# Kernel optimization log

Hardware: AMD Instinct MI355X
Metric: run time of the kernel (lower is better)

Reference implementation:

```python
import jax, jax.numpy as jnp
import numpy as np

RADIUS = 51  # odd-ified from 50
WEIGHT = 0.5
THRESHOLD = 10.0


def _gaussian_kernel_2d(k: int) -> np.ndarray:
    # Replicates cv2.getGaussianKernel(k, 0): sigma = 0.3*((k-1)*0.5 - 1) + 0.8
    sigma = 0.3 * ((k - 1) * 0.5 - 1.0) + 0.8
    x = np.arange(k, dtype=np.float64) - (k - 1) / 2.0
    g = np.exp(-(x ** 2) / (2.0 * sigma ** 2))
    g = g / g.sum()
    return np.outer(g, g).astype(np.float32)  # (k, k)


def filter2d(img, kernel):
    # img: (b, c, h, w), kernel: (k, k); depthwise 'same' conv (symmetric zero pad)
    b, c, h, w = img.shape
    k = kernel.shape[-1]
    p = k // 2
    x = img.reshape(b * c, 1, h, w)
    w2 = kernel.reshape(1, 1, k, k).astype(img.dtype)
    out = jax.lax.conv_general_dilated(
        x, w2,
        window_strides=(1, 1),
        padding=[(p, p), (p, p)],
        dimension_numbers=("NCHW", "OIHW", "NCHW"),
    )
    return out.reshape(b, c, h, w)


def setup_inputs() -> dict:
    key = jax.random.key(0)
    img = jax.random.uniform(key, (16, 3, 512, 512), dtype=jnp.float32)
    kernel = jnp.asarray(_gaussian_kernel_2d(RADIUS))
    return {"img": img, "kernel": kernel}


def reference(img, kernel):
    blur = filter2d(img, kernel)
    residual = img - blur
    mask = (jnp.abs(residual) * 255.0 > THRESHOLD).astype(img.dtype)
    soft_mask = filter2d(mask, kernel)
    sharp = jnp.clip(img + WEIGHT * residual, 0.0, 1.0)
    return soft_mask * sharp + (1.0 - soft_mask) * img
```

## Files before the change

kernel.cpp:

```cpp
#include <hip/hip_runtime.h>
#include <hip/hip_fp16.h>
#include <math.h>

#define IMG_H 512
#define IMG_W 512
#define NCH   48
#define KR    51
#define WEIGHT 0.5f
#define MASK_BITS 0x2905

typedef _Float16 f16x8 __attribute__((ext_vector_type(8)));
typedef float    f32x4 __attribute__((ext_vector_type(4)));

struct GK { float g[KR]; };

__device__ __forceinline__ f16x8 band_frag(const unsigned short* tbl, int delta,
                                           int lane) {
  union { f16x8 v; unsigned short s[8]; } r;
  const int base = delta + 63 - (lane & 15) + 4 * (lane >> 4);
  #pragma unroll
  for (int e = 0; e < 8; ++e)
    r.s[e] = tbl[base + (e & 3) + 16 * (e >> 2)];
  return r.v;
}

__device__ __forceinline__ int swz1536(int b) { return (b & 7) * 192 + (b >> 3); }

template <int MODE>
__global__ __launch_bounds__(256) void hpass(const void* __restrict__ inp,
                                             __half* __restrict__ outp, GK gk) {
  __shared__ unsigned short tbl[128];
  const int tid = threadIdx.x;
  if (tid < 128) {
    int j = tid - 38;
    float v = (j >= 0 && j < KR) ? gk.g[j] : 0.f;
    tbl[tid] = __half_as_ushort(__float2half(v));
  }
  __syncthreads();
  const int lane = tid & 63;
  const int w    = tid >> 6;
  const int r0   = blockIdx.x * 16;
  const int x0   = w * 128;
  const int row  = r0 + (lane & 15);
  const int g4   = 4 * (lane >> 4);

  f16x8 bf[6];
  #pragma unroll
  for (int d = 0; d < 6; ++d) bf[d] = band_frag(tbl, 16 * d - 48, lane);

  f32x4 acc[8];
  #pragma unroll
  for (int n = 0; n < 8; ++n) acc[n] = (f32x4){0.f, 0.f, 0.f, 0.f};

  #pragma unroll
  for (int n = 0; n < 8; ++n) {
    #pragma unroll
    for (int i = 0; i < 3; ++i) {
      const int D  = 32 * (((16 * n - 25) >> 5) + i) - 16 * n;
      const int kb = x0 + 16 * n + D;
      if (kb >= 0 && kb < IMG_W) {
        union { f16x8 v; _Float16 h[8]; unsigned short s[8]; } a;
        if (MODE == 0) {
          const float* pr = (const float*)inp + (size_t)row * IMG_W + kb + g4;
          float4 lo = *reinterpret_cast<const float4*>(pr);
          float4 hi = *reinterpret_cast<const float4*>(pr + 16);
          a.h[0] = (_Float16)lo.x; a.h[1] = (_Float16)lo.y;
          a.h[2] = (_Float16)lo.z; a.h[3] = (_Float16)lo.w;
          a.h[4] = (_Float16)hi.x; a.h[5] = (_Float16)hi.y;
          a.h[6] = (_Float16)hi.z; a.h[7] = (_Float16)hi.w;
        } else {
          const unsigned short* pr =
              (const unsigned short*)inp + (size_t)row * IMG_W + kb + g4;
          uint2 lo = *reinterpret_cast<const uint2*>(pr);
          uint2 hi = *reinterpret_cast<const uint2*>(pr + 16);
          unsigned short sv[8] = {
            (unsigned short)(lo.x), (unsigned short)(lo.x >> 16),
            (unsigned short)(lo.y), (unsigned short)(lo.y >> 16),
            (unsigned short)(hi.x), (unsigned short)(hi.x >> 16),
            (unsigned short)(hi.y), (unsigned short)(hi.y >> 16) };
          #pragma unroll
          for (int e = 0; e < 8; ++e)
            a.s[e] = ((sv[e] & 0x7fff) > MASK_BITS) ? 0x3C00 : 0;
        }
        const int bi = (n & 1) ? 2 * i : 2 * i + 1;
        acc[n] = __builtin_amdgcn_mfma_f32_16x16x32_f16(a.v, bf[bi], acc[n],
                                                        0, 0, 0);
      }
    }
  }
  const int q = 4 * (lane >> 4);
  #pragma unroll
  for (int n = 0; n < 8; ++n) {
    const int col = x0 + 16 * n + (lane & 15);
    #pragma unroll
    for (int j = 0; j < 4; ++j)
      outp[(size_t)(r0 + q + j) * IMG_W + col] = __float2half(acc[n][j]);
  }
}

template <int FINAL>
__global__ __launch_bounds__(256) void vpass(const __half* __restrict__ tin,
                                             const float* __restrict__ img,
                                             const __half* __restrict__ resv,
                                             void* __restrict__ outp, GK gk) {
  __shared__ unsigned short tbl[128];
  const int tid = threadIdx.x;
  if (tid < 128) {
    int j = tid - 38;
    float v = (j >= 0 && j < KR) ? gk.g[j] : 0.f;
    tbl[tid] = __half_as_ushort(__float2half(v));
  }
  __syncthreads();
  const int lane = tid & 63;
  const int w    = tid >> 6;
  const int b    = swz1536(blockIdx.x);
  const int c    = b >> 5;
  const int yb   = (b >> 2) & 7;
  const int xb   = b & 3;
  const int ybw  = yb * 64 + 32 * (w >> 1);
  const int x0   = xb * 128 + 64 * (w & 1);
  const size_t plane = (size_t)c * IMG_H * IMG_W;

  f16x8 bf[6];
  #pragma unroll
  for (int d = 0; d < 6; ++d) bf[d] = band_frag(tbl, 16 * d - 48, lane);

  f32x4 acc[2][4];
  #pragma unroll
  for (int yt = 0; yt < 2; ++yt)
    #pragma unroll
    for (int xt = 0; xt < 4; ++xt) acc[yt][xt] = (f32x4){0.f, 0.f, 0.f, 0.f};

  const int g4 = 4 * (lane >> 4);
  #pragma unroll
  for (int xt = 0; xt < 4; ++xt) {
    const int colg = x0 + 16 * xt + (lane & 15);
    #pragma unroll
    for (int i = 0; i < 3; ++i) {
      const int k0 = ybw + 32 * (i - 1);
      if (k0 >= 0 && k0 < IMG_H) {
        const unsigned short* pB =
            (const unsigned short*)tin + plane + (size_t)(k0 + g4) * IMG_W + colg;
        union { f16x8 v; unsigned short s[8]; } bv;
        #pragma unroll
        for (int e = 0; e < 8; ++e)
          bv.s[e] = pB[(size_t)((e & 3) + 16 * (e >> 2)) * IMG_W];
        acc[0][xt] = __builtin_amdgcn_mfma_f32_16x16x32_f16(bf[2 * i + 1], bv.v,
                                                            acc[0][xt], 0, 0, 0);
        acc[1][xt] = __builtin_amdgcn_mfma_f32_16x16x32_f16(bf[2 * i],     bv.v,
                                                            acc[1][xt], 0, 0, 0);
      }
    }
  }
  #pragma unroll
  for (int yt = 0; yt < 2; ++yt) {
    #pragma unroll
    for (int xt = 0; xt < 4; ++xt) {
      const int y0 = ybw + 16 * yt + g4;
      const int xc = x0 + 16 * xt + (lane & 15);
      #pragma unroll
      for (int j = 0; j < 4; ++j) {
        const size_t off = plane + (size_t)(y0 + j) * IMG_W + xc;
        const float bl = acc[yt][xt][j];
        const float iv = img[off];
        if (FINAL) {
          const float r = __half2float(resv[off]);
          const float sharp = fminf(fmaxf(fmaf(WEIGHT, r, iv), 0.f), 1.f);
          ((float*)outp)[off] = fmaf(bl, sharp - iv, iv);
        } else {
          ((__half*)outp)[off] = __float2half(iv - bl);
        }
      }
    }
  }
}

extern "C" void kernel_launch(void* const* d_in, const int* in_sizes, int n_in,
                              void* d_out, int out_size, void* d_ws, size_t ws_size,
                              hipStream_t stream) {
  const float* img = (const float*)d_in[0];
  GK gk;
  {
    double sigma = 0.3 * ((KR - 1) * 0.5 - 1.0) + 0.8;
    double gs[KR], sum = 0.0;
    for (int i = 0; i < KR; ++i) {
      double xd = (double)i - (KR - 1) / 2.0;
      gs[i] = exp(-(xd * xd) / (2.0 * sigma * sigma));
      sum += gs[i];
    }
    for (int i = 0; i < KR; ++i) gk.g[i] = (float)(gs[i] / sum);
  }

  const size_t npx = (size_t)NCH * IMG_H * IMG_W;
  __half* t1  = (__half*)d_out;
  __half* res = (__half*)d_ws;
  __half* t2  = (__half*)((char*)d_ws + npx * sizeof(__half));

  const int hgrid = NCH * IMG_H / 16;
  const int vgrid = NCH * (IMG_H / 64) * (IMG_W / 128);

  hpass<0><<<hgrid, 256, 0, stream>>>(img, t1, gk);
  vpass<0><<<vgrid, 256, 0, stream>>>(t1, img, res , res, gk);
  hpass<1><<<hgrid, 256, 0, stream>>>(res, t2, gk);
  vpass<1><<<vgrid, 256, 0, stream>>>(t2, img, res, d_out, gk);
}
```

Measured before the change: 207.1 us.

## Fuse horizontal and vertical blur passes into one kernel per stage

Merges the separable horizontal and vertical MFMA passes into a single kernel per blur stage. Each wave computes horizontal blur for a 128-row halo strip of a 16-column slice, keeps the fp16 results in registers, and feeds them directly as the B operand of the vertical MFMA. This removes the intermediate t1/t2 global round-trips and two launches. In exchange, each tile recomputes horizontal blur over the vertical halo (128 rows for 64 output rows), roughly doubling horizontal MFMA work and input reads.

```diff
diff --git a/kernel.cpp b/kernel.cpp
--- a/kernel.cpp
+++ b/kernel.cpp
@@ -10,6 +10,7 @@
 #define MASK_BITS 0x2905
 
 typedef _Float16 f16x8 __attribute__((ext_vector_type(8)));
+typedef _Float16 f16x4 __attribute__((ext_vector_type(4)));
 typedef float    f32x4 __attribute__((ext_vector_type(4)));
 
 struct GK { float g[KR]; };
@@ -24,11 +25,12 @@
   return r.v;
 }
 
-__device__ __forceinline__ int swz1536(int b) { return (b & 7) * 192 + (b >> 3); }
+__device__ __forceinline__ int swz3072(int b) { return (b & 7) * 384 + (b >> 3); }
 
-template <int MODE>
-__global__ __launch_bounds__(256) void hpass(const void* __restrict__ inp,
-                                             __half* __restrict__ outp, GK gk) {
+template <int PASS>
+__global__ __launch_bounds__(256) void fusedhv(const float* __restrict__ img,
+                                               const __half* __restrict__ resv,
+                                               void* __restrict__ outp, GK gk) {
   __shared__ unsigned short tbl[128];
   const int tid = threadIdx.x;
   if (tid < 128) {
@@ -37,139 +39,108 @@
     tbl[tid] = __half_as_ushort(__float2half(v));
   }
   __syncthreads();
+
   const int lane = tid & 63;
   const int w    = tid >> 6;
-  const int r0   = blockIdx.x * 16;
-  const int x0   = w * 128;
-  const int row  = r0 + (lane & 15);
-  const int g4   = 4 * (lane >> 4);
+  const int b    = swz3072(blockIdx.x);
+  const int c    = b >> 6;
+  const int yb   = (b >> 3) & 7;
+  const int xb   = b & 7;
+  const int y0   = yb * 64;
+  const int xw   = xb * 64 + 16 * w;
+  const size_t plane = (size_t)c * IMG_H * IMG_W;
+  const int l15 = lane & 15;
+  const int g4  = 4 * (lane >> 4);
 
   f16x8 bf[6];
   #pragma unroll
   for (int d = 0; d < 6; ++d) bf[d] = band_frag(tbl, 16 * d - 48, lane);
 
-  f32x4 acc[8];
+  const bool podd = (xw >> 4) & 1;
+  f16x8 bh[3];
   #pragma unroll
-  for (int n = 0; n < 8; ++n) acc[n] = (f32x4){0.f, 0.f, 0.f, 0.f};
+  for (int i = 0; i < 3; ++i) bh[i] = podd ? bf[2 * i] : bf[2 * i + 1];
+
+  const int kb0 = ((xw - 25) >> 5) * 32;
+
+  f16x4 h16[8];
+  #pragma unroll
+  for (int ch = 0; ch < 8; ++ch) {
+    f32x4 acc = {0.f, 0.f, 0.f, 0.f};
+    const int r0 = y0 - 32 + 16 * ch;
+    if (r0 >= 0 && r0 < IMG_H) {
+      const size_t rowoff = plane + (size_t)(r0 + l15) * IMG_W;
+      #pragma unroll
+      for (int i = 0; i < 3; ++i) {
+        const int kb = kb0 + 32 * i;
+        if (kb >= 0 && kb < IMG_W) {
+          union { f16x8 v; _Float16 h[8]; unsigned short s[8]; } a;
+          if (PASS == 0) {
+            const float* pr = img + rowoff + kb + g4;
+            float4 lo = *reinterpret_cast<const float4*>(pr);
+            float4 hi = *reinterpret_cast<const float4*>(pr + 16);
+            a.h[0] = (_Float16)lo.x; a.h[1] = (_Float16)lo.y;
+            a.h[2] = (_Float16)lo.z; a.h[3] = (_Float16)lo.w;
+            a.h[4] = (_Float16)hi.x; a.h[5] = (_Float16)hi.y;
+            a.h[6] = (_Float16)hi.z; a.h[7] = (_Float16)hi.w;
+          } else {
+            const unsigned short* pr =
+                (const unsigned short*)resv + rowoff + kb + g4;
+            uint2 lo = *reinterpret_cast<const uint2*>(pr);
+            uint2 hi = *reinterpret_cast<const uint2*>(pr + 16);
+            unsigned short sv[8] = {
+              (unsigned short)lo.x, (unsigned short)(lo.x >> 16),
+              (unsigned short)lo.y, (unsigned short)(lo.y >> 16),
+              (unsigned short)hi.x, (unsigned short)(hi.x >> 16),
+              (unsigned short)hi.y, (unsigned short)(hi.y >> 16) };
+            #pragma unroll
+            for (int e = 0; e < 8; ++e)
+              a.s[e] = ((sv[e] & 0x7fff) > MASK_BITS) ? 0x3C00 : 0;
+          }
+          acc = __builtin_amdgcn_mfma_f32_16x16x32_f16(a.v, bh[i], acc, 0, 0, 0);
+        }
+      }
+    }
+    f16x4 hq;
+    hq[0] = (_Float16)acc[0]; hq[1] = (_Float16)acc[1];
+    hq[2] = (_Float16)acc[2]; hq[3] = (_Float16)acc[3];
+    h16[ch] = hq;
+  }
+
+  f32x4 accv[4];
+  #pragma unroll
+  for (int yc = 0; yc < 4; ++yc) accv[yc] = (f32x4){0.f, 0.f, 0.f, 0.f};
+  #pragma unroll
+  for (int yc = 0; yc < 4; ++yc) {
+    #pragma unroll
+    for (int i = 0; i < 3; ++i) {
+      const int kr = ((16 * yc - 25) >> 5) + i;
+      const int ci = 2 * kr + 2;
+      union { f16x8 v; f16x4 q[2]; } bv;
+      bv.q[0] = h16[ci]; bv.q[1] = h16[ci + 1];
+      if (yc & 1)
+        accv[yc] = __builtin_amdgcn_mfma_f32_16x16x32_f16(bf[2 * i], bv.v,
+                                                          accv[yc], 0, 0, 0);
+      else
+        accv[yc] = __builtin_amdgcn_mfma_f32_16x16x32_f16(bf[2 * i + 1], bv.v,
+                                                          accv[yc], 0, 0, 0);
+    }
+  }
 
   #pragma unroll
-  for (int n = 0; n < 8; ++n) {
+  for (int yc = 0; yc < 4; ++yc) {
     #pragma unroll
-    for (int i = 0; i < 3; ++i) {
-      const int D  = 32 * (((16 * n - 25) >> 5) + i) - 16 * n;
-      const int kb = x0 + 16 * n + D;
-      if (kb >= 0 && kb < IMG_W) {
-        union { f16x8 v; _Float16 h[8]; unsigned short s[8]; } a;
-        if (MODE == 0) {
-          const float* pr = (const float*)inp + (size_t)row * IMG_W + kb + g4;
-          float4 lo = *reinterpret_cast<const float4*>(pr);
-          float4 hi = *reinterpret_cast<const float4*>(pr + 16);
-          a.h[0] = (_Float16)lo.x; a.h[1] = (_Float16)lo.y;
-          a.h[2] = (_Float16)lo.z; a.h[3] = (_Float16)lo.w;
-          a.h[4] = (_Float16)hi.x; a.h[5] = (_Float16)hi.y;
-          a.h[6] = (_Float16)hi.z; a.h[7] = (_Float16)hi.w;
-        } else {
-          const unsigned short* pr =
-              (const unsigned short*)inp + (size_t)row * IMG_W + kb + g4;
-          uint2 lo = *reinterpret_cast<const uint2*>(pr);
-          uint2 hi = *reinterpret_cast<const uint2*>(pr + 16);
-          unsigned short sv[8] = {
-            (unsigned short)(lo.x), (unsigned short)(lo.x >> 16),
-            (unsigned short)(lo.y), (unsigned short)(lo.y >> 16),
-            (unsigned short)(hi.x), (unsigned short)(hi.x >> 16),
-            (unsigned short)(hi.y), (unsigned short)(hi.y >> 16) };
-          #pragma unroll
-          for (int e = 0; e < 8; ++e)
-            a.s[e] = ((sv[e] & 0x7fff) > MASK_BITS) ? 0x3C00 : 0;
-        }
-        const int bi = (n & 1) ? 2 * i : 2 * i + 1;
-        acc[n] = __builtin_amdgcn_mfma_f32_16x16x32_f16(a.v, bf[bi], acc[n],
-                                                        0, 0, 0);
-      }
-    }
-  }
-  const int q = 4 * (lane >> 4);
-  #pragma unroll
-  for (int n = 0; n < 8; ++n) {
-    const int col = x0 + 16 * n + (lane & 15);
-    #pragma unroll
-    for (int j = 0; j < 4; ++j)
-      outp[(size_t)(r0 + q + j) * IMG_W + col] = __float2half(acc[n][j]);
-  }
-}
-
-template <int FINAL>
-__global__ __launch_bounds__(256) void vpass(const __half* __restrict__ tin,
-                                             const float* __restrict__ img,
-                                             const __half* __restrict__ resv,
-                                             void* __restrict__ outp, GK gk) {
-  __shared__ unsigned short tbl[128];
-  const int tid = threadIdx.x;
-  if (tid < 128) {
-    int j = tid - 38;
-    float v = (j >= 0 && j < KR) ? gk.g[j] : 0.f;
-    tbl[tid] = __half_as_ushort(__float2half(v));
-  }
-  __syncthreads();
-  const int lane = tid & 63;
-  const int w    = tid >> 6;
-  const int b    = swz1536(blockIdx.x);
-  const int c    = b >> 5;
-  const int yb   = (b >> 2) & 7;
-  const int xb   = b & 3;
-  const int ybw  = yb * 64 + 32 * (w >> 1);
-  const int x0   = xb * 128 + 64 * (w & 1);
-  const size_t plane = (size_t)c * IMG_H * IMG_W;
-
-  f16x8 bf[6];
-  #pragma unroll
-  for (int d = 0; d < 6; ++d) bf[d] = band_frag(tbl, 16 * d - 48, lane);
-
-  f32x4 acc[2][4];
-  #pragma unroll
-  for (int yt = 0; yt < 2; ++yt)
-    #pragma unroll
-    for (int xt = 0; xt < 4; ++xt) acc[yt][xt] = (f32x4){0.f, 0.f, 0.f, 0.f};
-
-  const int g4 = 4 * (lane >> 4);
-  #pragma unroll
-  for (int xt = 0; xt < 4; ++xt) {
-    const int colg = x0 + 16 * xt + (lane & 15);
-    #pragma unroll
-    for (int i = 0; i < 3; ++i) {
-      const int k0 = ybw + 32 * (i - 1);
-      if (k0 >= 0 && k0 < IMG_H) {
-        const unsigned short* pB =
-            (const unsigned short*)tin + plane + (size_t)(k0 + g4) * IMG_W + colg;
-        union { f16x8 v; unsigned short s[8]; } bv;
-        #pragma unroll
-        for (int e = 0; e < 8; ++e)
-          bv.s[e] = pB[(size_t)((e & 3) + 16 * (e >> 2)) * IMG_W];
-        acc[0][xt] = __builtin_amdgcn_mfma_f32_16x16x32_f16(bf[2 * i + 1], bv.v,
-                                                            acc[0][xt], 0, 0, 0);
-        acc[1][xt] = __builtin_amdgcn_mfma_f32_16x16x32_f16(bf[2 * i],     bv.v,
-                                                            acc[1][xt], 0, 0, 0);
-      }
-    }
-  }
-  #pragma unroll
-  for (int yt = 0; yt < 2; ++yt) {
-    #pragma unroll
-    for (int xt = 0; xt < 4; ++xt) {
-      const int y0 = ybw + 16 * yt + g4;
-      const int xc = x0 + 16 * xt + (lane & 15);
-      #pragma unroll
-      for (int j = 0; j < 4; ++j) {
-        const size_t off = plane + (size_t)(y0 + j) * IMG_W + xc;
-        const float bl = acc[yt][xt][j];
-        const float iv = img[off];
-        if (FINAL) {
-          const float r = __half2float(resv[off]);
-          const float sharp = fminf(fmaxf(fmaf(WEIGHT, r, iv), 0.f), 1.f);
-          ((float*)outp)[off] = fmaf(bl, sharp - iv, iv);
-        } else {
-          ((__half*)outp)[off] = __float2half(iv - bl);
-        }
+    for (int j = 0; j < 4; ++j) {
+      const int y = y0 + 16 * yc + g4 + j;
+      const size_t off = plane + (size_t)y * IMG_W + xw + l15;
+      const float bl = accv[yc][j];
+      const float iv = img[off];
+      if (PASS == 0) {
+        ((__half*)outp)[off] = __float2half(iv - bl);
+      } else {
+        const float r = __half2float(resv[off]);
+        const float sharp = fminf(fmaxf(fmaf(WEIGHT, r, iv), 0.f), 1.f);
+        ((float*)outp)[off] = fmaf(bl, sharp - iv, iv);
       }
     }
   }
@@ -191,16 +162,10 @@
     for (int i = 0; i < KR; ++i) gk.g[i] = (float)(gs[i] / sum);
   }
 
-  const size_t npx = (size_t)NCH * IMG_H * IMG_W;
-  __half* t1  = (__half*)d_out;
   __half* res = (__half*)d_ws;
-  __half* t2  = (__half*)((char*)d_ws + npx * sizeof(__half));
 
-  const int hgrid = NCH * IMG_H / 16;
-  const int vgrid = NCH * (IMG_H / 64) * (IMG_W / 128);
+  const int grid = NCH * (IMG_H / 64) * (IMG_W / 64);
 
-  hpass<0><<<hgrid, 256, 0, stream>>>(img, t1, gk);
-  vpass<0><<<vgrid, 256, 0, stream>>>(t1, img, res , res, gk);
-  hpass<1><<<hgrid, 256, 0, stream>>>(res, t2, gk);
-  vpass<1><<<vgrid, 256, 0, stream>>>(t2, img, res, d_out, gk);
+  fusedhv<0><<<grid, 256, 0, stream>>>(img, res, res, gk);
+  fusedhv<1><<<grid, 256, 0, stream>>>(img, res, d_out, gk);
 }
```

New measurement: 258.0 us. 1.25x slower.
